# Performance work log

Hardware: AMD Instinct MI355X
Metric: run time of the kernel (lower is better)

The kernel has to match this reference:

```python
import jax, jax.numpy as jnp
import numpy as np


def setup_inputs() -> dict:
    key = jax.random.key(0)
    ks = jax.random.split(key, 5)
    B, c_in, c_out, style_d = 8, 128, 128, 512
    D = H = W = 32
    f = 3
    # xavier_uniform-like scale for conv weight
    fan_in = c_in * f * f * f
    fan_out = c_out * f * f * f
    limit = float(np.sqrt(6.0 / (fan_in + fan_out)))
    x = jax.random.normal(ks[0], (B, c_in, D, H, W), dtype=jnp.float32)
    s = jax.random.normal(ks[1], (B, style_d), dtype=jnp.float32)
    w = jax.random.uniform(ks[2], (c_out, c_in, f, f, f), dtype=jnp.float32, minval=-limit, maxval=limit)
    b = jnp.zeros((c_out, 1, 1, 1), dtype=jnp.float32)
    lim_a = float(np.sqrt(1.0 / style_d))
    affine_w = jax.random.uniform(ks[3], (c_in, style_d), dtype=jnp.float32, minval=-lim_a, maxval=lim_a)
    affine_b = jnp.zeros((c_in,), dtype=jnp.float32)
    return {"x": x, "s": s, "w": w, "b": b, "affine_w": affine_w, "affine_b": affine_b}


def _per_sample_conv(xi, wi):
    # xi: [c_in, D, H, W], wi: [c_out, c_in, 3, 3, 3]
    out = jax.lax.conv_general_dilated(
        xi[None],  # [1, c_in, D, H, W]
        wi,
        window_strides=(1, 1, 1),
        padding=((1, 1), (1, 1), (1, 1)),
        dimension_numbers=("NCDHW", "OIDHW", "NCDHW"),
    )
    return out[0]  # [c_out, D, H, W]


def reference(x, s, w, b, affine_w, affine_b):
    # Style -> per-sample channel scales
    style = s @ affine_w.T + affine_b  # [B, c_in]
    # Modulate: [B, c_out, c_in, f, f, f]
    wmod = w[None] * (style[:, None, :, None, None, None] + 1.0)
    # Demodulate
    d = jnp.sqrt(jnp.sum(jnp.square(wmod), axis=(2, 3, 4, 5), keepdims=True) + 1e-8)
    wmod = wmod / d
    # Per-sample conv (equivalent to grouped conv with groups=B)
    out = jax.vmap(_per_sample_conv)(x, wmod)  # [B, c_out, D, H, W]
    return out + b[None]
```

## Files before the change

### kernel.cpp

```cpp
#include <hip/hip_runtime.h>
#include <stdint.h>
#include <stddef.h>

typedef __attribute__((ext_vector_type(8))) short short8;
typedef __attribute__((ext_vector_type(4))) float floatx4;

#define CI 128
#define CO 128
#define SP 32768
#define BATCH 8
#define STYLED 512
#define KV 3456

typedef __attribute__((address_space(1))) const void gvoid_t;
typedef __attribute__((address_space(3))) void lvoid_t;

__device__ __forceinline__ void gload16(const void* g, void* l) {
    __builtin_amdgcn_global_load_lds((gvoid_t*)g, (lvoid_t*)l, 16, 0, 0);
}

__device__ __forceinline__ short f2bf(float f) {
    uint32_t u = __builtin_bit_cast(uint32_t, f);
    u = (u + 0x7FFFu + ((u >> 16) & 1u)) >> 16;
    return (short)(u & 0xFFFFu);
}

__global__ void k_style(const float* __restrict__ s, const float* __restrict__ aw,
                        const float* __restrict__ ab, float* __restrict__ m) {
    __shared__ float ssh[STYLED];
    int b = blockIdx.x;
    int i = threadIdx.x;
    for (int r = 0; r < STYLED / 128; ++r) ssh[r * 128 + i] = s[b * STYLED + r * 128 + i];
    __syncthreads();
    float acc = ab[i] + 1.0f;
    const float4* awr = (const float4*)(aw + (size_t)i * STYLED);
    for (int d4 = 0; d4 < STYLED / 4; ++d4) {
        float4 v = awr[d4];
        acc += v.x * ssh[d4 * 4] + v.y * ssh[d4 * 4 + 1] + v.z * ssh[d4 * 4 + 2] + v.w * ssh[d4 * 4 + 3];
    }
    m[b * CI + i] = acc;
}

__global__ void k_wmod(const float* __restrict__ w, const float* __restrict__ m,
                       short* __restrict__ wt) {
    int b = blockIdx.x >> 7;
    int o = blockIdx.x & 127;
    int lane = threadIdx.x;
    const float* wrow = w + (size_t)o * KV;
    const float* mrow = m + b * CI;
    float sum = 0.f;
    for (int e = lane; e < KV; e += 64) {
        int i = e / 27;
        float v = wrow[e] * mrow[i];
        sum += v * v;
    }
    #pragma unroll
    for (int off = 32; off >= 1; off >>= 1) sum += __shfl_xor(sum, off);
    float scale = 1.0f / sqrtf(sum + 1e-8f);
    int ophase = (o >> 1) & 3;
    for (int e = lane; e < KV; e += 64) {
        int i = e / 27;
        int k = e - i * 27;
        float v = wrow[e] * mrow[i] * scale;
        int c = i >> 5, il = i & 31, g = il >> 3, r = il & 7;
        int gl = g ^ ophase;
        wt[(((size_t)((b * 4 + c) * 27 + k)) * 128 + o) * 32 + gl * 8 + r] = f2bf(v);
    }
}

__global__ void k_xt(const float* __restrict__ x, short* __restrict__ xt) {
    __shared__ float t[128][33];
    int bid = blockIdx.x;
    int b = bid >> 10;
    int zy = bid & 1023;
    const float* src = x + (size_t)b * CI * SP + (size_t)zy * 32;
    int tid = threadIdx.x;
    int wlane = tid & 31, irow = tid >> 5;
    for (int it = 0; it < 16; ++it) {
        int i = it * 8 + irow;
        t[i][wlane] = src[(size_t)i * SP + wlane];
    }
    __syncthreads();
    short* dst = xt + ((size_t)(b * SP + zy * 32)) * CI;
    for (int it = 0; it < 2; ++it) {
        int idx = it * 256 + tid;
        int wv = idx >> 4, g = idx & 15;
        short8 v;
        #pragma unroll
        for (int j = 0; j < 8; ++j) v[j] = f2bf(t[g * 8 + j][wv]);
        *(short8*)(dst + (size_t)wv * CI + g * 8) = v;
    }
}

__launch_bounds__(512, 4)
__global__ void k_conv(const short* __restrict__ xt, const short* __restrict__ wt,
                       const float* __restrict__ bias, float* __restrict__ out,
                       const short* __restrict__ zeropage) {
    __shared__ short lds_x[816 * 32];
    __shared__ short lds_w[2][128 * 32];

    int bid = blockIdx.x;
    int b = bid & 7;
    int t = bid >> 3;
    int zt = t & 15, yt = t >> 4;
    int z0 = zt * 2, y0 = yt * 4;

    int tid = threadIdx.x;
    int lane = tid & 63;
    int wid = tid >> 6;
    int wm = wid >> 2;
    int wn = wid & 3;
    int l15 = lane & 15;
    int lhi = lane >> 4;

    floatx4 acc[4][4];
    #pragma unroll
    for (int a = 0; a < 4; ++a)
        #pragma unroll
        for (int c = 0; c < 4; ++c) acc[a][c] = (floatx4){0.f, 0.f, 0.f, 0.f};

    const short* wb = wt + (size_t)b * (4 * 27 * 128 * 32);
    const short* xb = xt + (size_t)b * SP * CI;

    for (int c = 0; c < 4; ++c) {
        for (int j = 0; ; ++j) {
            int s = wid + 8 * j;
            if (s >= 51) break;
            int G = s * 64 + lane;
            int rowid = G >> 2, g = G & 3;
            int zh = rowid / 204; int rr = rowid - zh * 204;
            int yh = rr / 34;     int wh = rr - yh * 34;
            int zz = z0 + zh - 1, yy = y0 + yh - 1, ww = wh - 1;
            int q = g ^ ((rowid >> 1) & 3);
            const short* src;
            if ((unsigned)zz < 32u && (unsigned)yy < 32u && (unsigned)ww < 32u)
                src = xb + ((size_t)(zz * 1024 + yy * 32 + ww)) * CI + c * 32 + q * 8;
            else
                src = zeropage + q * 8;
            gload16(src, (void*)((char*)lds_x + s * 1024));
        }
        gload16(wb + ((size_t)(c * 27 + 0)) * 4096 + wid * 512 + lane * 8,
                (void*)((char*)lds_w[0] + wid * 1024));
        __syncthreads();

        for (int tap = 0; tap < 27; ++tap) {
            int cur = tap & 1;
            if (tap < 26)
                gload16(wb + ((size_t)(c * 27 + tap + 1)) * 4096 + wid * 512 + lane * 8,
                        (void*)((char*)lds_w[cur ^ 1] + wid * 1024));
            int kd = tap / 9, r9 = tap - kd * 9;
            int kh = r9 / 3, kw = r9 - kh * 3;

            short8 af[4];
            #pragma unroll
            for (int mf = 0; mf < 4; ++mf) {
                int o = wm * 64 + mf * 16 + l15;
                af[mf] = *(const short8*)((const char*)lds_w[cur] + o * 64 +
                                          ((lhi ^ ((o >> 1) & 3)) << 4));
            }
            #pragma unroll
            for (int nf = 0; nf < 4; ++nf) {
                int n = wn * 64 + nf * 16;
                int zi = n >> 7, yi = (n >> 5) & 3;
                int h = ((zi + kd) * 6 + (yi + kh)) * 34 + (n & 31) + kw + l15;
                short8 bf = *(const short8*)((const char*)lds_x + h * 64 +
                                             ((lhi ^ ((h >> 1) & 3)) << 4));
                #pragma unroll
                for (int mf = 0; mf < 4; ++mf)
                    acc[mf][nf] = __builtin_amdgcn_mfma_f32_16x16x32_bf16(af[mf], bf, acc[mf][nf], 0, 0, 0);
            }
            __syncthreads();
        }
    }

    float bv[4][4];
    #pragma unroll
    for (int mf = 0; mf < 4; ++mf)
        #pragma unroll
        for (int j = 0; j < 4; ++j)
            bv[mf][j] = bias[wm * 64 + mf * 16 + lhi * 4 + j];

    #pragma unroll
    for (int mf = 0; mf < 4; ++mf) {
        int o = wm * 64 + mf * 16 + lhi * 4;
        #pragma unroll
        for (int nf = 0; nf < 4; ++nf) {
            int n = wn * 64 + nf * 16;
            int zi = n >> 7, yi = (n >> 5) & 3, wcol = (n & 31) + l15;
            size_t obase = ((size_t)(b * CO + o)) * SP + (size_t)(z0 + zi) * 1024 + (y0 + yi) * 32 + wcol;
            #pragma unroll
            for (int j = 0; j < 4; ++j)
                out[obase + (size_t)j * SP] = acc[mf][nf][j] + bv[mf][j];
        }
    }
}

extern "C" void kernel_launch(void* const* d_in, const int* in_sizes, int n_in,
                              void* d_out, int out_size, void* d_ws, size_t ws_size,
                              hipStream_t stream) {
    const float* x  = (const float*)d_in[0];
    const float* s  = (const float*)d_in[1];
    const float* w  = (const float*)d_in[2];
    const float* bb = (const float*)d_in[3];
    const float* aw = (const float*)d_in[4];
    const float* ab = (const float*)d_in[5];
    float* out = (float*)d_out;

    float* style_m = (float*)d_ws;
    short* wmodT   = (short*)((char*)d_ws + 4096);
    short* xT      = (short*)((char*)d_ws + 4096 + 7077888);
    short* zpage   = (short*)((char*)d_ws + 4096 + 7077888 + 67108864);

    hipMemsetAsync(zpage, 0, 256, stream);
    k_style<<<BATCH, 128, 0, stream>>>(s, aw, ab, style_m);
    k_wmod<<<BATCH * CO, 64, 0, stream>>>(w, style_m, wmodT);
    k_xt<<<BATCH * 1024, 256, 0, stream>>>(x, xT);
    k_conv<<<BATCH * 128, 512, 0, stream>>>(xT, wmodT, bb, out, zpage);
}
```

Before: 295.9 us.

## Triple-buffer conv weight taps with vmcnt waits; widen transpose tiles

The conv kernel's weight staging moves from a double buffer to a triple buffer with a prefetch distance of two taps. Each tap now ends with an explicit s_waitcnt vmcnt plus a raw s_barrier instead of __syncthreads, so one weight load can stay in flight across the barrier. Separately, the x transpose kernel processes 128-position tiles using float4 loads, converts to bf16 before writing LDS, and launches 4x fewer blocks. This adds LDS use in the conv kernel, which may lower occupancy, and relies on hand-managed vmcnt counting being correct.

```diff
diff --git a/kernel.cpp b/kernel.cpp
--- a/kernel.cpp
+++ b/kernel.cpp
@@ -69,26 +69,33 @@
 }
 
 __global__ void k_xt(const float* __restrict__ x, short* __restrict__ xt) {
-    __shared__ float t[128][33];
+    __shared__ short t[128 * 130 + 2];
     int bid = blockIdx.x;
-    int b = bid >> 10;
-    int zy = bid & 1023;
-    const float* src = x + (size_t)b * CI * SP + (size_t)zy * 32;
+    int b = bid >> 8;
+    int z = (bid >> 3) & 31;
+    int y0 = (bid & 7) * 4;
     int tid = threadIdx.x;
-    int wlane = tid & 31, irow = tid >> 5;
+    const float* src = x + (size_t)b * CI * SP + (size_t)z * 1024 + (size_t)y0 * 32;
+    int r8 = tid >> 5;
+    int s32 = tid & 31;
     for (int it = 0; it < 16; ++it) {
-        int i = it * 8 + irow;
-        t[i][wlane] = src[(size_t)i * SP + wlane];
+        int ch = it * 8 + r8;
+        float4 v = *(const float4*)(src + (size_t)ch * SP + s32 * 4);
+        uint32_t p0 = ((uint32_t)(uint16_t)f2bf(v.y) << 16) | (uint16_t)f2bf(v.x);
+        uint32_t p1 = ((uint32_t)(uint16_t)f2bf(v.w) << 16) | (uint16_t)f2bf(v.z);
+        uint32_t* row = (uint32_t*)&t[ch * 130 + s32 * 4];
+        row[0] = p0;
+        row[1] = p1;
     }
     __syncthreads();
-    short* dst = xt + ((size_t)(b * SP + zy * 32)) * CI;
-    for (int it = 0; it < 2; ++it) {
+    short* dstb = xt + ((size_t)(b * SP + z * 1024 + y0 * 32)) * CI;
+    for (int it = 0; it < 8; ++it) {
         int idx = it * 256 + tid;
-        int wv = idx >> 4, g = idx & 15;
+        int sp = idx >> 4, g = idx & 15;
         short8 v;
         #pragma unroll
-        for (int j = 0; j < 8; ++j) v[j] = f2bf(t[g * 8 + j][wv]);
-        *(short8*)(dst + (size_t)wv * CI + g * 8) = v;
+        for (int j = 0; j < 8; ++j) v[j] = t[(g * 8 + j) * 130 + sp];
+        *(short8*)(dstb + (size_t)sp * CI + g * 8) = v;
     }
 }
 
@@ -97,7 +104,9 @@
                        const float* __restrict__ bias, float* __restrict__ out,
                        const short* __restrict__ zeropage) {
     __shared__ short lds_x[816 * 32];
-    __shared__ short lds_w[2][128 * 32];
+    __shared__ short lds_w0[128 * 32];
+    __shared__ short lds_w1[128 * 32];
+    __shared__ short lds_w2[128 * 32];
 
     int bid = blockIdx.x;
     int b = bid & 7;
@@ -140,14 +149,21 @@
             gload16(src, (void*)((char*)lds_x + s * 1024));
         }
         gload16(wb + ((size_t)(c * 27 + 0)) * 4096 + wid * 512 + lane * 8,
-                (void*)((char*)lds_w[0] + wid * 1024));
-        __syncthreads();
+                (void*)((char*)lds_w0 + wid * 1024));
+        gload16(wb + ((size_t)(c * 27 + 1)) * 4096 + wid * 512 + lane * 8,
+                (void*)((char*)lds_w1 + wid * 1024));
+        asm volatile("s_waitcnt vmcnt(1)" ::: "memory");
+        __builtin_amdgcn_s_barrier();
+        asm volatile("" ::: "memory");
+
+        short* wcur = lds_w0;
+        short* wnx1 = lds_w1;
+        short* wnx2 = lds_w2;
 
         for (int tap = 0; tap < 27; ++tap) {
-            int cur = tap & 1;
-            if (tap < 26)
-                gload16(wb + ((size_t)(c * 27 + tap + 1)) * 4096 + wid * 512 + lane * 8,
-                        (void*)((char*)lds_w[cur ^ 1] + wid * 1024));
+            if (tap < 25)
+                gload16(wb + ((size_t)(c * 27 + tap + 2)) * 4096 + wid * 512 + lane * 8,
+                        (void*)((char*)wnx2 + wid * 1024));
             int kd = tap / 9, r9 = tap - kd * 9;
             int kh = r9 / 3, kw = r9 - kh * 3;
 
@@ -155,7 +171,7 @@
             #pragma unroll
             for (int mf = 0; mf < 4; ++mf) {
                 int o = wm * 64 + mf * 16 + l15;
-                af[mf] = *(const short8*)((const char*)lds_w[cur] + o * 64 +
+                af[mf] = *(const short8*)((const char*)wcur + o * 64 +
                                           ((lhi ^ ((o >> 1) & 3)) << 4));
             }
             #pragma unroll
@@ -169,7 +185,13 @@
                 for (int mf = 0; mf < 4; ++mf)
                     acc[mf][nf] = __builtin_amdgcn_mfma_f32_16x16x32_bf16(af[mf], bf, acc[mf][nf], 0, 0, 0);
             }
-            __syncthreads();
+
+            if (tap < 25)       asm volatile("s_waitcnt vmcnt(1)" ::: "memory");
+            else if (tap == 25) asm volatile("s_waitcnt vmcnt(0)" ::: "memory");
+            __builtin_amdgcn_s_barrier();
+            asm volatile("" ::: "memory");
+
+            short* tmp = wcur; wcur = wnx1; wnx1 = wnx2; wnx2 = tmp;
         }
     }
 
@@ -214,6 +236,6 @@
     hipMemsetAsync(zpage, 0, 256, stream);
     k_style<<<BATCH, 128, 0, stream>>>(s, aw, ab, style_m);
     k_wmod<<<BATCH * CO, 64, 0, stream>>>(w, style_m, wmodT);
-    k_xt<<<BATCH * 1024, 256, 0, stream>>>(x, xT);
+    k_xt<<<BATCH * 32 * 8, 256, 0, stream>>>(x, xT);
     k_conv<<<BATCH * 128, 512, 0, stream>>>(xT, wmodT, bb, out, zpage);
 }
```

Result: no change. 297.5 us (+0.5%).
